# Kernel tuning notes

Measured on AMD Instinct MI355X. Metric: run time of the kernel, lower is better.

Reference implementation:

```python
import jax, jax.numpy as jnp
import numpy as np

# Hyperparameters matching the torch module instantiation
STRIDE = (2, 2, 2)
PADDING = (1, 1, 1)
OUTPUT_PADDING = (1, 1, 1)
DILATION = (2, 2, 2)
KERNEL = (3, 3, 3)


def setup_inputs() -> dict:
    key = jax.random.key(0)
    k1, k2, k3 = jax.random.split(key, 3)
    x = jax.random.normal(k1, (2, 64, 32, 32, 32), dtype=jnp.float32)
    # torch ConvTranspose3d weight layout: (C_in, C_out//groups, kD, kH, kW)
    weight = jax.random.normal(k2, (64, 32, 3, 3, 3), dtype=jnp.float32) * 0.05
    bias = jax.random.normal(k3, (32,), dtype=jnp.float32) * 0.05
    return {"x": x, "weight": weight, "bias": bias}


def reference(x, weight, bias):
    # Same math as the naive torch module: zero-insertion upsample by stride,
    # symmetric pad by dilation*(k-1)-padding, dense conv3d with the spatially
    # flipped weight at rhs dilation, trailing output_padding, then bias add.
    # lhs_dilation performs the zero-insertion implicitly (identical result).
    pad = tuple(max(0, d * (k - 1) - p)
                for d, k, p in zip(DILATION, KERNEL, PADDING))
    # (C_in, C_out, k,k,k) -> (C_out, C_in, k,k,k), flipped spatially
    w = jnp.flip(jnp.transpose(weight, (1, 0, 2, 3, 4)), axis=(2, 3, 4))
    out = jax.lax.conv_general_dilated(
        x, w,
        window_strides=(1, 1, 1),
        padding=[(p, p) for p in pad],
        lhs_dilation=STRIDE,
        rhs_dilation=DILATION,
        dimension_numbers=("NCDHW", "OIDHW", "NCDHW"),
    )
    opd, oph, opw = OUTPUT_PADDING
    out = jnp.pad(out, ((0, 0), (0, 0), (0, opd), (0, oph), (0, opw)))
    return out + bias[None, :, None, None, None]
```

## Files before the change

kernel.cpp:

```cpp
#include <hip/hip_runtime.h>


#define DOUT 66
#define PL (DOUT*DOUT)
#define ROW_B 4352
#define IDG_B (6*ROW_B)

typedef _Float16 half8   __attribute__((ext_vector_type(8)));
typedef float    floatx16 __attribute__((ext_vector_type(16)));
typedef float    floatx4  __attribute__((ext_vector_type(4)));

__global__ void __launch_bounds__(256) wprep(const float* __restrict__ w,
                                             _Float16* __restrict__ wA)
{
    int o = blockIdx.x * 256 + threadIdx.x;
    int j = o & 7;
    int tmp = o >> 3;
    int lane = tmp & 63;
    int g = tmp >> 6;
    int cc = g / 27, tap = g - cc * 27;
    int co = lane & 31, khalf = lane >> 5;
    int ci = cc * 16 + khalf * 8 + j;
    wA[o] = (_Float16)w[ci * 864 + co * 27 + tap];
}

__global__ void __launch_bounds__(256, 2) convt(
    const float* __restrict__ x, const _Float16* __restrict__ wA,
    const float* __restrict__ bias, float* __restrict__ out)
{
    __shared__ __align__(16) unsigned char xlds[3 * IDG_B];

    const int tid  = threadIdx.x;
    const int lane = tid & 63;
    const int wv   = tid >> 6;

    unsigned b = blockIdx.x;
    const unsigned xcd = b & 7u;
    const int n     = (int)(xcd & 1u);
    const unsigned rest = b >> 3;
    const int hpg   = (int)((xcd >> 1) * 2 + (rest & 1u));
    const int dp    = (int)(rest >> 1);
    const int hpb   = hpg * 4;

    const float* xn = x + (size_t)n * 2097152;

    {
        for (int t = tid; t < 1152; t += 256) {
            const int r   = t >> 6;
            const int ccg = (t >> 3) & 7;
            const int gq  = t & 7;
            const int id_l = r / 6, ihl = r - 6 * id_l;
            const int id = dp - 1 + id_l;
            const int ih = hpb - 1 + ihl;
            unsigned char* dst = xlds + (id_l * 6 + ihl) * ROW_B
                               + ccg * 544 + (gq * 4 + 1) * 16;
            if (((unsigned)id < 32u) & ((unsigned)ih < 32u)) {
                const float* src = xn + ccg * 262144 + (id * 32 + ih) * 32 + gq * 4;
                floatx4 f[8];
                #pragma unroll
                for (int j = 0; j < 8; ++j) f[j] = *(const floatx4*)(src + j * 32768);
                #pragma unroll
                for (int m = 0; m < 4; ++m) {
                    unsigned p0 = __builtin_bit_cast(unsigned,
                        __builtin_amdgcn_cvt_pkrtz(f[0][m], f[1][m]));
                    unsigned p1 = __builtin_bit_cast(unsigned,
                        __builtin_amdgcn_cvt_pkrtz(f[2][m], f[3][m]));
                    unsigned p2 = __builtin_bit_cast(unsigned,
                        __builtin_amdgcn_cvt_pkrtz(f[4][m], f[5][m]));
                    unsigned p3 = __builtin_bit_cast(unsigned,
                        __builtin_amdgcn_cvt_pkrtz(f[6][m], f[7][m]));
                    *(uint4*)(dst + m * 16) = make_uint4(p0, p1, p2, p3);
                }
            } else {
                #pragma unroll
                for (int m = 0; m < 4; ++m)
                    *(uint4*)(dst + m * 16) = make_uint4(0, 0, 0, 0);
            }
        }
        for (int h = tid; h < 288; h += 256) {
            const int r = h >> 4, rem = h & 15;
            const int cg = rem >> 1, side = rem & 1;
            *(uint4*)(xlds + r * ROW_B + cg * 544 + (side ? 33 * 16 : 0)) =
                make_uint4(0, 0, 0, 0);
        }
    }
    __syncthreads();

    const int wp    = lane & 31;
    const int khalf = lane >> 5;

    floatx16 acc = {};
    #pragma unroll
    for (int cc = 0; cc < 4; ++cc) {
        uint4 A[27];
        const _Float16* wl = wA + ((size_t)cc * 27 * 64 + lane) * 8;
        #pragma unroll
        for (int t = 0; t < 27; ++t) A[t] = *(const uint4*)(wl + t * 512);
        const int cb = (2 * cc + khalf) * 544 + wp * 16;
        #pragma unroll
        for (int kd = 0; kd < 3; ++kd)
        #pragma unroll
        for (int kh = 0; kh < 3; ++kh)
        #pragma unroll
        for (int kw = 0; kw < 3; ++kw) {
            const int tap = (kd * 3 + kh) * 3 + kw;
            const uint4* bp = (const uint4*)(xlds
                + ((2 - kd) * 6 + (wv + 2 - kh)) * ROW_B + cb + (2 - kw) * 16);
            acc = __builtin_amdgcn_mfma_f32_32x32x16_f16(
                __builtin_bit_cast(half8, A[tap]),
                __builtin_bit_cast(half8, bp[0]), acc, 0, 0, 0);
        }
    }

    __syncthreads();
    float* val = (float*)xlds;
    #pragma unroll
    for (int r = 0; r < 16; ++r) {
        const int co = (r & 3) + 8 * (r >> 2) + 4 * khalf;
        val[((size_t)wv * 32 + co) * 33 + wp] = acc[r];
    }
    __syncthreads();


    const int NQ = (hpg == 7) ? 165 : 132;

    #pragma unroll
    for (int c = 0; c < 8; ++c) {
        const int co = wv * 8 + c;
        const float bw = bias[co];
        const floatx4 bb = {bw, bw, bw, bw};
        float* pc = out + (size_t)(n * 32 + co) * ((size_t)DOUT * PL)
                    + 8 * hpg * DOUT;

        {
            float* eb = pc + (size_t)(2 * dp) * PL;
            for (int q = lane; q < NQ; q += 64)
                *(floatx4*)(eb + 4 * q) = bb;
        }
        {
            float* ob = pc + (size_t)(2 * dp + 1) * PL;
            for (int q = lane; q < NQ; q += 64) {
                floatx4 o;
                #pragma unroll
                for (int j = 0; j < 4; ++j) {
                    const int e = 4 * q + j;
                    const int rl = e / 66;
                    const int ow = e - rl * 66;
                    float v = bw;
                    if ((rl & 1) && rl < 8 && (ow & 1) && ow < 65)
                        v += val[(((rl >> 1) * 32) + co) * 33 + (ow >> 1)];
                    o[j] = v;
                }
                *(floatx4*)(ob + 4 * q) = o;
            }
        }
        if (dp == 31) {
            float* p64 = pc + (size_t)64 * PL;
            for (int q = lane; q < NQ; q += 64)
                *(floatx4*)(p64 + 4 * q) = bb;
            float* p65 = pc + (size_t)65 * PL;
            for (int q = lane; q < NQ; q += 64)
                *(floatx4*)(p65 + 4 * q) = bb;
        }
    }
}

extern "C" void kernel_launch(void* const* d_in, const int* in_sizes, int n_in,
                              void* d_out, int out_size, void* d_ws, size_t ws_size,
                              hipStream_t stream) {
    const float* x    = (const float*)d_in[0];
    const float* wgt  = (const float*)d_in[1];
    const float* bias = (const float*)d_in[2];
    float* out = (float*)d_out;
    _Float16* wA = (_Float16*)d_ws;

    wprep<<<216, 256, 0, stream>>>(wgt, wA);
    convt<<<512, 256, 0, stream>>>(x, wA, bias, out);
}
```

Baseline: 110.7 us.

## Split fused conv-transpose into MFMA conv kernel and separate full-plane expand kernel

The conv kernel now writes its compact 32x32x32 results to a workspace instead of scattering them into the strided output itself. A new expand kernel, launched with one block per output plane, fills each 66x66 plane with bias and adds the dense values at odd positions using contiguous vector stores. The aim is to spread the large, output-bound write across many more blocks than the 512 conv blocks could issue. In exchange it adds an extra kernel launch and an intermediate buffer that is written and then read back from global memory.

```diff
diff --git a/kernel.cpp b/kernel.cpp
--- a/kernel.cpp
+++ b/kernel.cpp
@@ -5,6 +5,7 @@
 #define PL (DOUT*DOUT)
 #define ROW_B 4352
 #define IDG_B (6*ROW_B)
+#define VAL_OFF 131072
 
 typedef _Float16 half8   __attribute__((ext_vector_type(8)));
 typedef float    floatx16 __attribute__((ext_vector_type(16)));
@@ -24,9 +25,9 @@
     wA[o] = (_Float16)w[ci * 864 + co * 27 + tap];
 }
 
-__global__ void __launch_bounds__(256, 2) convt(
+__global__ void __launch_bounds__(256, 2) conv_c(
     const float* __restrict__ x, const _Float16* __restrict__ wA,
-    const float* __restrict__ bias, float* __restrict__ out)
+    float* __restrict__ val_ws)
 {
     __shared__ __align__(16) unsigned char xlds[3 * IDG_B];
 
@@ -112,56 +113,55 @@
         }
     }
 
-    __syncthreads();
-    float* val = (float*)xlds;
-    #pragma unroll
-    for (int r = 0; r < 16; ++r) {
-        const int co = (r & 3) + 8 * (r >> 2) + 4 * khalf;
-        val[((size_t)wv * 32 + co) * 33 + wp] = acc[r];
+    __builtin_amdgcn_sched_barrier(0);
+    {
+        const int hp = hpb + wv;
+        #pragma unroll
+        for (int r = 0; r < 16; ++r) {
+            const int co = (r & 3) + 8 * (r >> 2) + 4 * khalf;
+            val_ws[((((size_t)(n * 32 + co)) * 32 + dp) * 32 + hp) * 32 + wp]
+                = acc[r];
+        }
     }
-    __syncthreads();
+}
 
+__global__ void __launch_bounds__(256) expand(
+    const float* __restrict__ val_ws, const float* __restrict__ bias,
+    float* __restrict__ out)
+{
+    __shared__ float v[1024];
 
-    const int NQ = (hpg == 7) ? 165 : 132;
+    const int tid = threadIdx.x;
+    const unsigned b = blockIdx.x;
+    const int nco = (int)(b & 63u);
+    const int od  = (int)(b >> 6);
 
-    #pragma unroll
-    for (int c = 0; c < 8; ++c) {
-        const int co = wv * 8 + c;
-        const float bw = bias[co];
-        const floatx4 bb = {bw, bw, bw, bw};
-        float* pc = out + (size_t)(n * 32 + co) * ((size_t)DOUT * PL)
-                    + 8 * hpg * DOUT;
+    const float bv = bias[nco & 31];
+    const floatx4 bb = {bv, bv, bv, bv};
+    float* plane = out + ((size_t)nco * DOUT + od) * PL;
 
-        {
-            float* eb = pc + (size_t)(2 * dp) * PL;
-            for (int q = lane; q < NQ; q += 64)
-                *(floatx4*)(eb + 4 * q) = bb;
+    const bool vplane = (od & 1) && (od < 65);
+    if (vplane) {
+        const float* src = val_ws + ((size_t)nco * 32 + (od >> 1)) * 1024;
+        ((floatx4*)v)[tid] = ((const floatx4*)src)[tid];
+        __syncthreads();
+        for (int q = tid; q < 1089; q += 256) {
+            const int e = 4 * q;
+            const int rl0 = e / 66;
+            const int ow0 = e - rl0 * 66;
+            floatx4 o = bb;
+            #pragma unroll
+            for (int j = 0; j < 4; ++j) {
+                int rr = rl0, ow = ow0 + j;
+                if (ow >= 66) { ow -= 66; ++rr; }
+                if ((rr & 1) && rr < 65 && (ow & 1) && ow < 64)
+                    o[j] += v[(rr >> 1) * 32 + (ow >> 1)];
+            }
+            *(floatx4*)(plane + e) = o;
         }
-        {
-            float* ob = pc + (size_t)(2 * dp + 1) * PL;
-            for (int q = lane; q < NQ; q += 64) {
-                floatx4 o;
-                #pragma unroll
-                for (int j = 0; j < 4; ++j) {
-                    const int e = 4 * q + j;
-                    const int rl = e / 66;
-                    const int ow = e - rl * 66;
-                    float v = bw;
-                    if ((rl & 1) && rl < 8 && (ow & 1) && ow < 65)
-                        v += val[(((rl >> 1) * 32) + co) * 33 + (ow >> 1)];
-                    o[j] = v;
-                }
-                *(floatx4*)(ob + 4 * q) = o;
-            }
-        }
-        if (dp == 31) {
-            float* p64 = pc + (size_t)64 * PL;
-            for (int q = lane; q < NQ; q += 64)
-                *(floatx4*)(p64 + 4 * q) = bb;
-            float* p65 = pc + (size_t)65 * PL;
-            for (int q = lane; q < NQ; q += 64)
-                *(floatx4*)(p65 + 4 * q) = bb;
-        }
+    } else {
+        for (int q = tid; q < 1089; q += 256)
+            *(floatx4*)(plane + 4 * q) = bb;
     }
 }
 
@@ -172,8 +172,10 @@
     const float* wgt  = (const float*)d_in[1];
     const float* bias = (const float*)d_in[2];
     float* out = (float*)d_out;
-    _Float16* wA = (_Float16*)d_ws;
+    _Float16* wA   = (_Float16*)d_ws;
+    float* val_ws  = (float*)((char*)d_ws + VAL_OFF);
 
     wprep<<<216, 256, 0, stream>>>(wgt, wA);
-    convt<<<512, 256, 0, stream>>>(x, wA, bias, out);
+    conv_c<<<512, 256, 0, stream>>>(x, wA, val_ws);
+    expand<<<4224, 256, 0, stream>>>(val_ws, bias, out);
 }
```

After: 112.4 us. Within noise of the previous version (+1.5%).
